# Kernel optimization log

Hardware: AMD Instinct MI355X
Metric: run time of the kernel (lower is better)

## Reference

```python
import jax, jax.numpy as jnp
import numpy as np

DIM_MODEL = 512
HEADS = 8
DIM_HEAD = 64
HIDDEN = HEADS * DIM_HEAD
SCALE = DIM_HEAD ** -0.5
GN_EPS = 1e-5


def setup_inputs() -> dict:
    key = jax.random.key(0)
    ks = jax.random.split(key, 7)
    b, t = 8, 4096
    x = jax.random.normal(ks[0], (b, DIM_MODEL, t), dtype=jnp.float32)
    mask = jax.random.randint(ks[1], (b, t), 0, 2) == 1  # bool padding mask
    # 1x1 convs are plain channel matmuls; kernels squeezed to 2D
    w_qkv = jax.random.normal(ks[2], (3 * HIDDEN, DIM_MODEL), dtype=jnp.float32) * (DIM_MODEL ** -0.5)
    w_out = jax.random.normal(ks[3], (DIM_MODEL, HIDDEN), dtype=jnp.float32) * (HIDDEN ** -0.5)
    b_out = jax.random.normal(ks[4], (DIM_MODEL,), dtype=jnp.float32) * 0.01
    gn_gamma = jnp.ones((DIM_MODEL,), dtype=jnp.float32)
    gn_beta = jnp.zeros((DIM_MODEL,), dtype=jnp.float32)
    return {"x": x, "mask": mask, "w_qkv": w_qkv, "w_out": w_out,
            "b_out": b_out, "gn_gamma": gn_gamma, "gn_beta": gn_beta}


def reference(x, mask, w_qkv, w_out, b_out, gn_gamma, gn_beta):
    b, c, t = x.shape
    # to_qkv: 1x1 conv == channel matmul -> [b, 3*hidden, t]
    qkv = jnp.einsum('oc,bct->bot', w_qkv, x)
    q, k, v = jnp.split(qkv, 3, axis=1)
    # 'b (h d) t -> b h d t'
    q = q.reshape(b, HEADS, DIM_HEAD, t)
    k = k.reshape(b, HEADS, DIM_HEAD, t)
    v = v.reshape(b, HEADS, DIM_HEAD, t)
    # additive mask: 0.0 where True, 1e-12 where False; broadcast 'b t -> b 1 1 t'
    maskf = jnp.where(mask, 0.0, 1e-12)[:, None, None, :].astype(x.dtype)
    q = jax.nn.softmax(q, axis=-2) * SCALE            # softmax over feature dim d
    k = jax.nn.softmax(k + maskf, axis=-1)            # softmax over time dim t
    # linear attention: O(t * d * e)
    context = jnp.einsum('bhdn,bhen->bhde', k, v)      # [b, h, d, e]
    out = jnp.einsum('bhde,bhdn->bhen', context, q)    # [b, h, e, t]
    out = out.reshape(b, HIDDEN, t)                    # 'b h e t -> b (h e) t'
    # to_out: 1x1 conv with bias, then GroupNorm(1, dim_model)
    y = jnp.einsum('oc,bct->bot', w_out, out) + b_out[None, :, None]
    mu = jnp.mean(y, axis=(1, 2), keepdims=True)
    var = jnp.var(y, axis=(1, 2), keepdims=True)
    y = (y - mu) * jax.lax.rsqrt(var + GN_EPS)
    return y * gn_gamma[None, :, None] + gn_beta[None, :, None]
```

## Files before the change

### kernel.cpp

```cpp
#include <hip/hip_runtime.h>
#include <stdint.h>

typedef unsigned short u16;
using f32x4 = __attribute__((ext_vector_type(4))) float;
using s16x8 = __attribute__((ext_vector_type(8))) short;

#define MFMA_BF16(a, b, c) __builtin_amdgcn_mfma_f32_16x16x32_bf16((a), (b), (c), 0, 0, 0)

#define GLOAD_LDS16(gptr, lptr)                                                               \
  __builtin_amdgcn_global_load_lds((const __attribute__((address_space(1))) uint32_t*)(gptr), \
                                   (__attribute__((address_space(3))) uint32_t*)(lptr), 16, 0, 0)

__device__ __forceinline__ u16 f2bf(float f) {
  union { float f; uint32_t u; } v; v.f = f;
  uint32_t r = v.u + 0x7fffu + ((v.u >> 16) & 1u);
  return (u16)(r >> 16);
}
__device__ __forceinline__ float bf2f(u16 h) {
  union { uint32_t u; float f; } v; v.u = ((uint32_t)h) << 16;
  return v.f;
}

__global__ void k_convert_w(const float* __restrict__ wq, const float* __restrict__ wo,
                            u16* __restrict__ wqb, u16* __restrict__ wob) {
  int i = blockIdx.x * 256 + threadIdx.x;
  const int nq = 1536 * 512 / 4;
  const int no = 512 * 512 / 4;
  if (i < nq) {
    float4 v = ((const float4*)wq)[i];
    u16* o = wqb + i * 4;
    o[0] = f2bf(v.x); o[1] = f2bf(v.y); o[2] = f2bf(v.z); o[3] = f2bf(v.w);
  } else if (i < nq + no) {
    int j = i - nq;
    float4 v = ((const float4*)wo)[j];
    u16* o = wob + j * 4;
    o[0] = f2bf(v.x); o[1] = f2bf(v.y); o[2] = f2bf(v.z); o[3] = f2bf(v.w);
  }
}

__global__ void k_transpose_x(const float* __restrict__ x, u16* __restrict__ xT) {
  __shared__ u16 tile[64][65];
  int b = blockIdx.z, c0 = blockIdx.y * 64, t0 = blockIdx.x * 64;
  const float* xp = x + ((size_t)b * 512 + c0) * 4096 + t0;
#pragma unroll
  for (int i = 0; i < 16; ++i) {
    int idx = threadIdx.x + i * 256;
    int r = idx >> 6, col = idx & 63;
    tile[r][col] = f2bf(xp[(size_t)r * 4096 + col]);
  }
  __syncthreads();
  u16* op = xT + ((size_t)b * 4096 + t0) * 512 + c0;
#pragma unroll
  for (int i = 0; i < 16; ++i) {
    int idx = threadIdx.x + i * 256;
    int r = idx >> 6, col = idx & 63;
    op[(size_t)r * 512 + col] = tile[col][r];
  }
}

__launch_bounds__(256, 2)
__global__ void k_gemm_qkv(const u16* __restrict__ A, const u16* __restrict__ BT,
                           u16* __restrict__ C, u16* __restrict__ qT) {
  __shared__ s16x8 As8[1024];
  __shared__ s16x8 Bs8[1024];
  int b = blockIdx.z;
  int m0 = blockIdx.y * 128, n0 = blockIdx.x * 128;
  const u16* Ab = A + (size_t)m0 * 512;
  const u16* Bb = BT + ((size_t)b * 4096 + n0) * 512;
  int tid = threadIdx.x, w = tid >> 6, lane = tid & 63;
  int wm = (w >> 1) * 64, wn = (w & 1) * 64;
  f32x4 acc[4][4] = {};
  for (int kt = 0; kt < 8; ++kt) {
    if (kt) __syncthreads();
#pragma unroll
    for (int it = 0; it < 4; ++it) {
      int L = (w * 4 + it) * 64 + lane;
      int r = L >> 3;
      int lc = (L & 7) ^ (r & 7);
      GLOAD_LDS16(Ab + (size_t)r * 512 + kt * 64 + lc * 8, ((char*)As8) + (w * 4 + it) * 1024);
      GLOAD_LDS16(Bb + (size_t)r * 512 + kt * 64 + lc * 8, ((char*)Bs8) + (w * 4 + it) * 1024);
    }
    asm volatile("s_waitcnt vmcnt(0)");
    __syncthreads();
#pragma unroll
    for (int kk = 0; kk < 2; ++kk) {
      int cb = kk * 4 + (lane >> 4);
      s16x8 af[4], bfr[4];
#pragma unroll
      for (int mi = 0; mi < 4; ++mi) {
        int r = wm + mi * 16 + (lane & 15);
        af[mi] = As8[r * 8 + (cb ^ (r & 7))];
      }
#pragma unroll
      for (int ni = 0; ni < 4; ++ni) {
        int r = wn + ni * 16 + (lane & 15);
        bfr[ni] = Bs8[r * 8 + (cb ^ (r & 7))];
      }
#pragma unroll
      for (int mi = 0; mi < 4; ++mi)
#pragma unroll
        for (int ni = 0; ni < 4; ++ni)
          acc[mi][ni] = MFMA_BF16(af[mi], bfr[ni], acc[mi][ni]);
    }
  }
  if (blockIdx.y < 4) {
    int head = (m0 >> 6) + (wm >> 6);
    int bh = b * 8 + head;
#pragma unroll
    for (int ni = 0; ni < 4; ++ni) {
      float mx = -1e30f;
#pragma unroll
      for (int mi = 0; mi < 4; ++mi)
#pragma unroll
        for (int j = 0; j < 4; ++j) mx = fmaxf(mx, acc[mi][ni][j]);
      mx = fmaxf(mx, __shfl_xor(mx, 16));
      mx = fmaxf(mx, __shfl_xor(mx, 32));
      float e[4][4];
      float s = 0.f;
#pragma unroll
      for (int mi = 0; mi < 4; ++mi)
#pragma unroll
        for (int j = 0; j < 4; ++j) { e[mi][j] = __expf(acc[mi][ni][j] - mx); s += e[mi][j]; }
      s += __shfl_xor(s, 16);
      s += __shfl_xor(s, 32);
      float sc = 0.125f / s;
      int t = n0 + wn + ni * 16 + (lane & 15);
      u16* op = qT + ((size_t)bh * 4096 + t) * 64 + (lane >> 4) * 4;
#pragma unroll
      for (int mi = 0; mi < 4; ++mi) {
        union { u16 u[4]; uint2 v; } pk;
#pragma unroll
        for (int j = 0; j < 4; ++j) pk.u[j] = f2bf(e[mi][j] * sc);
        *(uint2*)(op + mi * 16) = pk.v;
      }
    }
  } else {
    u16* Cb = C + ((size_t)b * 1536 + m0) * 4096 + n0;
#pragma unroll
    for (int mi = 0; mi < 4; ++mi)
#pragma unroll
      for (int ni = 0; ni < 4; ++ni)
#pragma unroll
        for (int j = 0; j < 4; ++j) {
          int mm = wm + mi * 16 + (lane >> 4) * 4 + j;
          int nn = wn + ni * 16 + (lane & 15);
          Cb[(size_t)mm * 4096 + nn] = f2bf(acc[mi][ni][j]);
        }
  }
}

__global__ void k_context_part(const u16* __restrict__ qkv, float* __restrict__ ctxp,
                               float* __restrict__ spart) {
  int s = blockIdx.x, bh = blockIdx.y;
  int b = bh >> 3, h = bh & 7;
  int w = threadIdx.x >> 6, lane = threadIdx.x & 63;
  int hi = lane >> 4, lo = lane & 15;
  const u16* vb = qkv + ((size_t)b * 1536 + 1024 + h * 64) * 4096 + s * 256;
  const u16* kb = qkv + ((size_t)b * 1536 + 512 + h * 64) * 4096 + s * 256;
  int d = w * 16 + lo;
  f32x4 acc[4] = {};
  float ssum = 0.f;
#pragma unroll
  for (int st = 0; st < 8; ++st) {
    int nn = st * 32 + hi * 8;
    s16x8 braw = *(const s16x8*)(kb + (size_t)d * 4096 + nn);
    s16x8 bexp;
#pragma unroll
    for (int j = 0; j < 8; ++j) {
      float f = __expf(bf2f((u16)braw[j]));
      ssum += f;
      bexp[j] = (short)f2bf(f);
    }
#pragma unroll
    for (int ei = 0; ei < 4; ++ei) {
      s16x8 a = *(const s16x8*)(vb + (size_t)(ei * 16 + lo) * 4096 + nn);
      acc[ei] = MFMA_BF16(a, bexp, acc[ei]);
    }
  }
  float* cp = ctxp + ((size_t)bh * 16 + s) * 4096;
#pragma unroll
  for (int ei = 0; ei < 4; ++ei) {
    float4 o;
    o.x = acc[ei][0]; o.y = acc[ei][1]; o.z = acc[ei][2]; o.w = acc[ei][3];
    *(float4*)&cp[(size_t)d * 64 + ei * 16 + hi * 4] = o;
  }
  ssum += __shfl_xor(ssum, 16);
  ssum += __shfl_xor(ssum, 32);
  if (lane < 16) spart[((size_t)bh * 16 + s) * 64 + w * 16 + lane] = ssum;
}

__global__ void k_ctx_reduce(const float* __restrict__ ctxp, const float* __restrict__ spart,
                             u16* __restrict__ Bg) {
  int q = blockIdx.x, bh = blockIdx.y;
  __shared__ float sinv[4];
  int tid = threadIdx.x;
  if (tid < 4) {
    int d = q * 4 + tid;
    float s = 0.f;
#pragma unroll
    for (int si = 0; si < 16; ++si) s += spart[((size_t)bh * 16 + si) * 64 + d];
    sinv[tid] = 1.f / s;
  }
  __syncthreads();
  int pos = q * 256 + tid;
  float v = 0.f;
#pragma unroll
  for (int si = 0; si < 16; ++si) v += ctxp[((size_t)bh * 16 + si) * 4096 + pos];
  Bg[(size_t)bh * 4096 + pos] = f2bf(v * sinv[(pos >> 6) & 3]);
}

__global__ void k_wfused(const u16* __restrict__ wout, const u16* __restrict__ Bg,
                         u16* __restrict__ Wf) {
  int bh = blockIdx.x;
  int b = bh >> 3, h = bh & 7;
  int w = threadIdx.x >> 6, lane = threadIdx.x & 63;
  int hi = lane >> 4, lo = lane & 15;
  const u16* Bb = Bg + (size_t)bh * 4096;
  const u16* Ab = wout + (size_t)h * 64;
  f32x4 acc[8][4] = {};
#pragma unroll
  for (int ks = 0; ks < 2; ++ks) {
    s16x8 bfr[4];
#pragma unroll
    for (int ni = 0; ni < 4; ++ni)
      bfr[ni] = *(const s16x8*)(Bb + (size_t)(ni * 16 + lo) * 64 + ks * 32 + hi * 8);
#pragma unroll
    for (int mi = 0; mi < 8; ++mi) {
      s16x8 a = *(const s16x8*)(Ab + (size_t)(w * 128 + mi * 16 + lo) * 512 + ks * 32 + hi * 8);
#pragma unroll
      for (int ni = 0; ni < 4; ++ni) acc[mi][ni] = MFMA_BF16(a, bfr[ni], acc[mi][ni]);
    }
  }
#pragma unroll
  for (int mi = 0; mi < 8; ++mi)
#pragma unroll
    for (int ni = 0; ni < 4; ++ni) {
      int m = w * 128 + mi * 16 + hi * 4;
      int d = ni * 16 + lo;
#pragma unroll
      for (int j = 0; j < 4; ++j)
        Wf[((size_t)b * 512 + m + j) * 512 + h * 64 + d] = f2bf(acc[mi][ni][j]);
    }
}

__launch_bounds__(256, 2)
__global__ void k_gemm_final(const u16* __restrict__ Wf, const u16* __restrict__ qT,
                             u16* __restrict__ Ybf, const float* __restrict__ bias,
                             float2* __restrict__ part2) {
  __shared__ s16x8 As8[1024];
  __shared__ s16x8 Bs8[1024];
  int b = blockIdx.z;
  int m0 = blockIdx.y * 128, n0 = blockIdx.x * 128;
  const u16* Ab = Wf + ((size_t)b * 512 + m0) * 512;
  const u16* qTb = qT + (size_t)b * 8 * 4096 * 64;
  int tid = threadIdx.x, w = tid >> 6, lane = tid & 63;
  int wm = (w >> 1) * 64, wn = (w & 1) * 64;
  f32x4 acc[4][4] = {};
  for (int kt = 0; kt < 8; ++kt) {
    if (kt) __syncthreads();
#pragma unroll
    for (int it = 0; it < 4; ++it) {
      int L = (w * 4 + it) * 64 + lane;
      int r = L >> 3;
      int lc = (L & 7) ^ (r & 7);
      GLOAD_LDS16(Ab + (size_t)r * 512 + kt * 64 + lc * 8, ((char*)As8) + (w * 4 + it) * 1024);
      int G = kt * 8 + lc;
      GLOAD_LDS16(qTb + ((size_t)(G >> 3) * 4096 + n0 + r) * 64 + (G & 7) * 8,
                  ((char*)Bs8) + (w * 4 + it) * 1024);
    }
    asm volatile("s_waitcnt vmcnt(0)");
    __syncthreads();
#pragma unroll
    for (int kk = 0; kk < 2; ++kk) {
      int cb = kk * 4 + (lane >> 4);
      s16x8 af[4], bfr[4];
#pragma unroll
      for (int mi = 0; mi < 4; ++mi) {
        int r = wm + mi * 16 + (lane & 15);
        af[mi] = As8[r * 8 + (cb ^ (r & 7))];
      }
#pragma unroll
      for (int ni = 0; ni < 4; ++ni) {
        int r = wn + ni * 16 + (lane & 15);
        bfr[ni] = Bs8[r * 8 + (cb ^ (r & 7))];
      }
#pragma unroll
      for (int mi = 0; mi < 4; ++mi)
#pragma unroll
        for (int ni = 0; ni < 4; ++ni)
          acc[mi][ni] = MFMA_BF16(af[mi], bfr[ni], acc[mi][ni]);
    }
  }
  u16* Yb = Ybf + ((size_t)b * 512 + m0) * 4096 + n0;
  float sm = 0.f, ssm = 0.f;
#pragma unroll
  for (int mi = 0; mi < 4; ++mi)
#pragma unroll
    for (int j = 0; j < 4; ++j) {
      int mm = wm + mi * 16 + (lane >> 4) * 4 + j;
      float bo = bias[m0 + mm];
#pragma unroll
      for (int ni = 0; ni < 4; ++ni) {
        int nn = wn + ni * 16 + (lane & 15);
        float vv = acc[mi][ni][j] + bo;
        sm += vv;
        ssm += vv * vv;
        Yb[(size_t)mm * 4096 + nn] = f2bf(vv);
      }
    }
#pragma unroll
  for (int off = 32; off; off >>= 1) { sm += __shfl_xor(sm, off); ssm += __shfl_xor(ssm, off); }
  __shared__ float sr[4], ssr[4];
  if (lane == 0) { sr[w] = sm; ssr[w] = ssm; }
  __syncthreads();
  if (tid == 0) {
    float2 o;
    o.x = sr[0] + sr[1] + sr[2] + sr[3];
    o.y = ssr[0] + ssr[1] + ssr[2] + ssr[3];
    part2[((size_t)b * 4 + blockIdx.y) * 32 + blockIdx.x] = o;
  }
}

__global__ void k_gn_norm(const u16* __restrict__ ybf, float* __restrict__ y,
                          const float2* __restrict__ part2,
                          const float* __restrict__ gamma, const float* __restrict__ beta) {
  int b = blockIdx.y;
  float s = 0.f, ss = 0.f;
#pragma unroll 8
  for (int i = 0; i < 128; ++i) { float2 pp = part2[b * 128 + i]; s += pp.x; ss += pp.y; }
  const float N = 512.f * 4096.f;
  float mu = s / N;
  float var = ss / N - mu * mu;
  float rstd = rsqrtf(var + 1e-5f);
  size_t base = ((size_t)b << 21) + (size_t)blockIdx.x * 16384;
  const s16x8* ip = (const s16x8*)(ybf + base);
  float4* opf = (float4*)(y + base);
#pragma unroll
  for (int i = 0; i < 8; ++i) {
    int idx = threadIdx.x + i * 256;
    int loc = (int)(blockIdx.x * 16384) + idx * 8;
    int c = loc >> 12;
    float g = gamma[c] * rstd, bt = beta[c];
    s16x8 v = ip[idx];
    float4 o0, o1;
    o0.x = (bf2f((u16)v[0]) - mu) * g + bt;
    o0.y = (bf2f((u16)v[1]) - mu) * g + bt;
    o0.z = (bf2f((u16)v[2]) - mu) * g + bt;
    o0.w = (bf2f((u16)v[3]) - mu) * g + bt;
    o1.x = (bf2f((u16)v[4]) - mu) * g + bt;
    o1.y = (bf2f((u16)v[5]) - mu) * g + bt;
    o1.z = (bf2f((u16)v[6]) - mu) * g + bt;
    o1.w = (bf2f((u16)v[7]) - mu) * g + bt;
    opf[idx * 2] = o0;
    opf[idx * 2 + 1] = o1;
  }
}

extern "C" void kernel_launch(void* const* d_in, const int* in_sizes, int n_in,
                              void* d_out, int out_size, void* d_ws, size_t ws_size,
                              hipStream_t stream) {
  const float* x     = (const float*)d_in[0];
  const float* wqkv  = (const float*)d_in[2];
  const float* wout  = (const float*)d_in[3];
  const float* bout  = (const float*)d_in[4];
  const float* gamma = (const float*)d_in[5];
  const float* beta  = (const float*)d_in[6];
  float* y = (float*)d_out;

  char* ws = (char*)d_ws;
  u16*    qkv_b = (u16*)ws;
  u16*    ybf   = (u16*)ws;
  u16*    xT    = (u16*)(ws + 100663296);
  float*  ctxp  = (float*)(ws + 100663296);
  float*  spart = (float*)(ws + 117440512);
  u16*    Bg    = (u16*)(ws + 117702656);
  u16*    qT    = (u16*)(ws + 134217728);
  u16*    wqkvb = (u16*)(ws + 167772160);
  u16*    woutb = (u16*)(ws + 169345024);
  u16*    Wfused= (u16*)(ws + 169869312);
  float2* part2 = (float2*)(ws + 174063616);

  k_convert_w<<<1024, 256, 0, stream>>>(wqkv, wout, wqkvb, woutb);
  {
    dim3 g(64, 8, 8);
    k_transpose_x<<<g, 256, 0, stream>>>(x, xT);
  }
  {
    dim3 g(32, 12, 8);
    k_gemm_qkv<<<g, 256, 0, stream>>>(wqkvb, xT, qkv_b, qT);
  }
  {
    dim3 g(16, 64);
    k_context_part<<<g, 256, 0, stream>>>(qkv_b, ctxp, spart);
  }
  {
    dim3 g(16, 64);
    k_ctx_reduce<<<g, 256, 0, stream>>>(ctxp, spart, Bg);
  }
  k_wfused<<<64, 256, 0, stream>>>(woutb, Bg, Wfused);
  {
    dim3 g(32, 4, 8);
    k_gemm_final<<<g, 256, 0, stream>>>(Wfused, qT, ybf, bout, part2);
  }
  {
    dim3 g(128, 8);
    k_gn_norm<<<g, 256, 0, stream>>>(ybf, y, part2, gamma, beta);
  }
}
```

Before: 177.9 us.

## Triple-buffer GEMM K-loop with 8-wave 128x256 tiles for QKV and final GEMMs

Replaces the synchronous single-buffer K loop in both big GEMMs with a shared macro that uses 8 waves, 128x256 output tiles and a three-stage LDS ring. Loads for tile kt+2 are issued while MFMAs run on tile kt, with s_setprio raised around the MFMA blocks. The aim is to hide global load latency and cut the wait-then-sync stalls. In exchange the kernels use 144KB of dynamic LDS, which allows only one block per CU, and the grid is halved, so the GroupNorm partial-sum count drops to 64 per batch.

```diff
diff --git a/kernel.cpp b/kernel.cpp
--- a/kernel.cpp
+++ b/kernel.cpp
@@ -58,53 +58,111 @@
   }
 }
 
-__launch_bounds__(256, 2)
+#define GEMM8W_CORE(ABASE, BSRC)                                                      \
+  s16x8* Asl = (s16x8*)lds;                             \
+  s16x8* Bsl = (s16x8*)(lds + 49152);                   \
+  int tid = threadIdx.x, w = tid >> 6, lane = tid & 63;                               \
+  int wr = w >> 2, wc = w & 3;                                                        \
+  int hi = lane >> 4, lo = lane & 15;                                                 \
+  int rsu = tid >> 3, pc = tid & 7;                                                   \
+  int lcs = pc ^ (rsu & 7);                                                           \
+  f32x4 acc[4][4] = {};                                                               \
+  _Pragma("unroll")                                                                   \
+  for (int t = 0; t < 2; ++t) {                                                       \
+    _Pragma("unroll")                                                                 \
+    for (int u = 0; u < 2; ++u) {                                                     \
+      int rr = u * 64 + rsu;                                                          \
+      GLOAD_LDS16(ABASE + (size_t)rr * 512 + t * 64 + lcs * 8,                        \
+                  ((char*)Asl) + ((size_t)t * 1024 + rr * 8 + pc) * 16);              \
+    }                                                                                 \
+    _Pragma("unroll")                                                                 \
+    for (int u = 0; u < 4; ++u) {                                                     \
+      int rr = u * 64 + rsu;                                                          \
+      GLOAD_LDS16(BSRC(rr, t, lcs),                                                   \
+                  ((char*)Bsl) + ((size_t)t * 2048 + rr * 8 + pc) * 16);              \
+    }                                                                                 \
+  }                                                                                   \
+  for (int kt = 0; kt < 8; ++kt) {                                                    \
+    if (kt < 7) { asm volatile("s_waitcnt vmcnt(6)" ::: "memory"); }                  \
+    else        { asm volatile("s_waitcnt vmcnt(0)" ::: "memory"); }                  \
+    __builtin_amdgcn_s_barrier();                                                     \
+    int bufc = kt % 3, bufs = (kt + 2) % 3;                                           \
+    const s16x8* Ac = Asl + bufc * 1024;                                              \
+    const s16x8* Bc = Bsl + bufc * 2048;                                              \
+    bool st = (kt < 6);                                                               \
+    s16x8 af[4], bfr[4];                                                              \
+    _Pragma("unroll")                                                                 \
+    for (int mi = 0; mi < 4; ++mi) {                                                  \
+      int r = wr * 64 + mi * 16 + lo;                                                 \
+      af[mi] = Ac[r * 8 + (hi ^ (r & 7))];                                            \
+    }                                                                                 \
+    _Pragma("unroll")                                                                 \
+    for (int ni = 0; ni < 4; ++ni) {                                                  \
+      int r = wc * 64 + ni * 16 + lo;                                                 \
+      bfr[ni] = Bc[r * 8 + (hi ^ (r & 7))];                                           \
+    }                                                                                 \
+    if (st) {                                                                         \
+      _Pragma("unroll")                                                               \
+      for (int u = 0; u < 2; ++u) {                                                   \
+        int rr = u * 64 + rsu;                                                        \
+        GLOAD_LDS16(ABASE + (size_t)rr * 512 + (kt + 2) * 64 + lcs * 8,               \
+                    ((char*)Asl) + ((size_t)bufs * 1024 + rr * 8 + pc) * 16);         \
+      }                                                                               \
+      {                                                                               \
+        int rr = rsu;                                                                 \
+        GLOAD_LDS16(BSRC(rr, (kt + 2), lcs),                                          \
+                    ((char*)Bsl) + ((size_t)bufs * 2048 + rr * 8 + pc) * 16);         \
+      }                                                                               \
+    }                                                                                 \
+    __builtin_amdgcn_s_setprio(1);                                                    \
+    _Pragma("unroll")                                                                 \
+    for (int mi = 0; mi < 4; ++mi)                                                    \
+      _Pragma("unroll")                                                               \
+      for (int ni = 0; ni < 4; ++ni)                                                  \
+        acc[mi][ni] = MFMA_BF16(af[mi], bfr[ni], acc[mi][ni]);                        \
+    __builtin_amdgcn_s_setprio(0);                                                    \
+    __builtin_amdgcn_s_barrier();                                                     \
+    _Pragma("unroll")                                                                 \
+    for (int mi = 0; mi < 4; ++mi) {                                                  \
+      int r = wr * 64 + mi * 16 + lo;                                                 \
+      af[mi] = Ac[r * 8 + ((4 + hi) ^ (r & 7))];                                      \
+    }                                                                                 \
+    _Pragma("unroll")                                                                 \
+    for (int ni = 0; ni < 4; ++ni) {                                                  \
+      int r = wc * 64 + ni * 16 + lo;                                                 \
+      bfr[ni] = Bc[r * 8 + ((4 + hi) ^ (r & 7))];                                     \
+    }                                                                                 \
+    if (st) {                                                                         \
+      _Pragma("unroll")                                                               \
+      for (int u = 1; u < 4; ++u) {                                                   \
+        int rr = u * 64 + rsu;                                                        \
+        GLOAD_LDS16(BSRC(rr, (kt + 2), lcs),                                          \
+                    ((char*)Bsl) + ((size_t)bufs * 2048 + rr * 8 + pc) * 16);         \
+      }                                                                               \
+    }                                                                                 \
+    __builtin_amdgcn_s_setprio(1);                                                    \
+    _Pragma("unroll")                                                                 \
+    for (int mi = 0; mi < 4; ++mi)                                                    \
+      _Pragma("unroll")                                                               \
+      for (int ni = 0; ni < 4; ++ni)                                                  \
+        acc[mi][ni] = MFMA_BF16(af[mi], bfr[ni], acc[mi][ni]);                        \
+    __builtin_amdgcn_s_setprio(0);                                                    \
+  }
+
+#define BSRC_X(rr, ktile, lc) (Bb + (size_t)(rr) * 512 + (ktile) * 64 + (lc) * 8)
+#define BSRC_Q(rr, ktile, lc) (Bq + (size_t)(ktile) * 262144 + (size_t)(rr) * 64 + (lc) * 8)
+
+__launch_bounds__(512, 1)
 __global__ void k_gemm_qkv(const u16* __restrict__ A, const u16* __restrict__ BT,
                            u16* __restrict__ C, u16* __restrict__ qT) {
-  __shared__ s16x8 As8[1024];
-  __shared__ s16x8 Bs8[1024];
+  extern __shared__ char lds[];
   int b = blockIdx.z;
-  int m0 = blockIdx.y * 128, n0 = blockIdx.x * 128;
+  int m0 = blockIdx.y * 128, n0 = blockIdx.x * 256;
   const u16* Ab = A + (size_t)m0 * 512;
   const u16* Bb = BT + ((size_t)b * 4096 + n0) * 512;
-  int tid = threadIdx.x, w = tid >> 6, lane = tid & 63;
-  int wm = (w >> 1) * 64, wn = (w & 1) * 64;
-  f32x4 acc[4][4] = {};
-  for (int kt = 0; kt < 8; ++kt) {
-    if (kt) __syncthreads();
-#pragma unroll
-    for (int it = 0; it < 4; ++it) {
-      int L = (w * 4 + it) * 64 + lane;
-      int r = L >> 3;
-      int lc = (L & 7) ^ (r & 7);
-      GLOAD_LDS16(Ab + (size_t)r * 512 + kt * 64 + lc * 8, ((char*)As8) + (w * 4 + it) * 1024);
-      GLOAD_LDS16(Bb + (size_t)r * 512 + kt * 64 + lc * 8, ((char*)Bs8) + (w * 4 + it) * 1024);
-    }
-    asm volatile("s_waitcnt vmcnt(0)");
-    __syncthreads();
-#pragma unroll
-    for (int kk = 0; kk < 2; ++kk) {
-      int cb = kk * 4 + (lane >> 4);
-      s16x8 af[4], bfr[4];
-#pragma unroll
-      for (int mi = 0; mi < 4; ++mi) {
-        int r = wm + mi * 16 + (lane & 15);
-        af[mi] = As8[r * 8 + (cb ^ (r & 7))];
-      }
-#pragma unroll
-      for (int ni = 0; ni < 4; ++ni) {
-        int r = wn + ni * 16 + (lane & 15);
-        bfr[ni] = Bs8[r * 8 + (cb ^ (r & 7))];
-      }
-#pragma unroll
-      for (int mi = 0; mi < 4; ++mi)
-#pragma unroll
-        for (int ni = 0; ni < 4; ++ni)
-          acc[mi][ni] = MFMA_BF16(af[mi], bfr[ni], acc[mi][ni]);
-    }
-  }
+  GEMM8W_CORE(Ab, BSRC_X)
   if (blockIdx.y < 4) {
-    int head = (m0 >> 6) + (wm >> 6);
+    int head = (int)blockIdx.y * 2 + wr;
     int bh = b * 8 + head;
 #pragma unroll
     for (int ni = 0; ni < 4; ++ni) {
@@ -124,8 +182,8 @@
       s += __shfl_xor(s, 16);
       s += __shfl_xor(s, 32);
       float sc = 0.125f / s;
-      int t = n0 + wn + ni * 16 + (lane & 15);
-      u16* op = qT + ((size_t)bh * 4096 + t) * 64 + (lane >> 4) * 4;
+      int t = n0 + wc * 64 + ni * 16 + lo;
+      u16* op = qT + ((size_t)bh * 4096 + t) * 64 + hi * 4;
 #pragma unroll
       for (int mi = 0; mi < 4; ++mi) {
         union { u16 u[4]; uint2 v; } pk;
@@ -142,10 +200,53 @@
       for (int ni = 0; ni < 4; ++ni)
 #pragma unroll
         for (int j = 0; j < 4; ++j) {
-          int mm = wm + mi * 16 + (lane >> 4) * 4 + j;
-          int nn = wn + ni * 16 + (lane & 15);
+          int mm = wr * 64 + mi * 16 + hi * 4 + j;
+          int nn = wc * 64 + ni * 16 + lo;
           Cb[(size_t)mm * 4096 + nn] = f2bf(acc[mi][ni][j]);
         }
+  }
+}
+
+__launch_bounds__(512, 1)
+__global__ void k_gemm_final(const u16* __restrict__ Wf, const u16* __restrict__ qT,
+                             u16* __restrict__ Ybf, const float* __restrict__ bias,
+                             float2* __restrict__ part2) {
+  extern __shared__ char lds[];
+  int b = blockIdx.z;
+  int m0 = blockIdx.y * 128, n0 = blockIdx.x * 256;
+  const u16* Ab = Wf + ((size_t)b * 512 + m0) * 512;
+  const u16* Bq = qT + ((size_t)b * 8 * 4096 + n0) * 64;
+  GEMM8W_CORE(Ab, BSRC_Q)
+  u16* Yb = Ybf + ((size_t)b * 512 + m0) * 4096 + n0;
+  float sm = 0.f, ssm = 0.f;
+#pragma unroll
+  for (int mi = 0; mi < 4; ++mi)
+#pragma unroll
+    for (int j = 0; j < 4; ++j) {
+      int mm = wr * 64 + mi * 16 + hi * 4 + j;
+      float bo = bias[m0 + mm];
+#pragma unroll
+      for (int ni = 0; ni < 4; ++ni) {
+        int nn = wc * 64 + ni * 16 + lo;
+        float vv = acc[mi][ni][j] + bo;
+        sm += vv;
+        ssm += vv * vv;
+        Yb[(size_t)mm * 4096 + nn] = f2bf(vv);
+      }
+    }
+#pragma unroll
+  for (int off = 32; off; off >>= 1) { sm += __shfl_xor(sm, off); ssm += __shfl_xor(ssm, off); }
+  float* sr = (float*)lds;
+  float* ssr = sr + 8;
+  __syncthreads();
+  if (lane == 0) { sr[w] = sm; ssr[w] = ssm; }
+  __syncthreads();
+  if (tid == 0) {
+    float2 o;
+    o.x = 0.f; o.y = 0.f;
+#pragma unroll
+    for (int i = 0; i < 8; ++i) { o.x += sr[i]; o.y += ssr[i]; }
+    part2[((size_t)b * 4 + blockIdx.y) * 16 + blockIdx.x] = o;
   }
 }
 
@@ -243,91 +344,13 @@
     }
 }
 
-__launch_bounds__(256, 2)
-__global__ void k_gemm_final(const u16* __restrict__ Wf, const u16* __restrict__ qT,
-                             u16* __restrict__ Ybf, const float* __restrict__ bias,
-                             float2* __restrict__ part2) {
-  __shared__ s16x8 As8[1024];
-  __shared__ s16x8 Bs8[1024];
-  int b = blockIdx.z;
-  int m0 = blockIdx.y * 128, n0 = blockIdx.x * 128;
-  const u16* Ab = Wf + ((size_t)b * 512 + m0) * 512;
-  const u16* qTb = qT + (size_t)b * 8 * 4096 * 64;
-  int tid = threadIdx.x, w = tid >> 6, lane = tid & 63;
-  int wm = (w >> 1) * 64, wn = (w & 1) * 64;
-  f32x4 acc[4][4] = {};
-  for (int kt = 0; kt < 8; ++kt) {
-    if (kt) __syncthreads();
-#pragma unroll
-    for (int it = 0; it < 4; ++it) {
-      int L = (w * 4 + it) * 64 + lane;
-      int r = L >> 3;
-      int lc = (L & 7) ^ (r & 7);
-      GLOAD_LDS16(Ab + (size_t)r * 512 + kt * 64 + lc * 8, ((char*)As8) + (w * 4 + it) * 1024);
-      int G = kt * 8 + lc;
-      GLOAD_LDS16(qTb + ((size_t)(G >> 3) * 4096 + n0 + r) * 64 + (G & 7) * 8,
-                  ((char*)Bs8) + (w * 4 + it) * 1024);
-    }
-    asm volatile("s_waitcnt vmcnt(0)");
-    __syncthreads();
-#pragma unroll
-    for (int kk = 0; kk < 2; ++kk) {
-      int cb = kk * 4 + (lane >> 4);
-      s16x8 af[4], bfr[4];
-#pragma unroll
-      for (int mi = 0; mi < 4; ++mi) {
-        int r = wm + mi * 16 + (lane & 15);
-        af[mi] = As8[r * 8 + (cb ^ (r & 7))];
-      }
-#pragma unroll
-      for (int ni = 0; ni < 4; ++ni) {
-        int r = wn + ni * 16 + (lane & 15);
-        bfr[ni] = Bs8[r * 8 + (cb ^ (r & 7))];
-      }
-#pragma unroll
-      for (int mi = 0; mi < 4; ++mi)
-#pragma unroll
-        for (int ni = 0; ni < 4; ++ni)
-          acc[mi][ni] = MFMA_BF16(af[mi], bfr[ni], acc[mi][ni]);
-    }
-  }
-  u16* Yb = Ybf + ((size_t)b * 512 + m0) * 4096 + n0;
-  float sm = 0.f, ssm = 0.f;
-#pragma unroll
-  for (int mi = 0; mi < 4; ++mi)
-#pragma unroll
-    for (int j = 0; j < 4; ++j) {
-      int mm = wm + mi * 16 + (lane >> 4) * 4 + j;
-      float bo = bias[m0 + mm];
-#pragma unroll
-      for (int ni = 0; ni < 4; ++ni) {
-        int nn = wn + ni * 16 + (lane & 15);
-        float vv = acc[mi][ni][j] + bo;
-        sm += vv;
-        ssm += vv * vv;
-        Yb[(size_t)mm * 4096 + nn] = f2bf(vv);
-      }
-    }
-#pragma unroll
-  for (int off = 32; off; off >>= 1) { sm += __shfl_xor(sm, off); ssm += __shfl_xor(ssm, off); }
-  __shared__ float sr[4], ssr[4];
-  if (lane == 0) { sr[w] = sm; ssr[w] = ssm; }
-  __syncthreads();
-  if (tid == 0) {
-    float2 o;
-    o.x = sr[0] + sr[1] + sr[2] + sr[3];
-    o.y = ssr[0] + ssr[1] + ssr[2] + ssr[3];
-    part2[((size_t)b * 4 + blockIdx.y) * 32 + blockIdx.x] = o;
-  }
-}
-
 __global__ void k_gn_norm(const u16* __restrict__ ybf, float* __restrict__ y,
                           const float2* __restrict__ part2,
                           const float* __restrict__ gamma, const float* __restrict__ beta) {
   int b = blockIdx.y;
   float s = 0.f, ss = 0.f;
 #pragma unroll 8
-  for (int i = 0; i < 128; ++i) { float2 pp = part2[b * 128 + i]; s += pp.x; ss += pp.y; }
+  for (int i = 0; i < 64; ++i) { float2 pp = part2[b * 64 + i]; s += pp.x; ss += pp.y; }
   const float N = 512.f * 4096.f;
   float mu = s / N;
   float var = ss / N - mu * mu;
@@ -380,14 +403,20 @@
   u16*    Wfused= (u16*)(ws + 169869312);
   float2* part2 = (float2*)(ws + 174063616);
 
+  const int GEMM_LDS = 147456;
+  (void)hipFuncSetAttribute((const void*)k_gemm_qkv,
+                            hipFuncAttributeMaxDynamicSharedMemorySize, GEMM_LDS);
+  (void)hipFuncSetAttribute((const void*)k_gemm_final,
+                            hipFuncAttributeMaxDynamicSharedMemorySize, GEMM_LDS);
+
   k_convert_w<<<1024, 256, 0, stream>>>(wqkv, wout, wqkvb, woutb);
   {
     dim3 g(64, 8, 8);
     k_transpose_x<<<g, 256, 0, stream>>>(x, xT);
   }
   {
-    dim3 g(32, 12, 8);
-    k_gemm_qkv<<<g, 256, 0, stream>>>(wqkvb, xT, qkv_b, qT);
+    dim3 g(16, 12, 8);
+    k_gemm_qkv<<<g, 512, GEMM_LDS, stream>>>(wqkvb, xT, qkv_b, qT);
   }
   {
     dim3 g(16, 64);
@@ -399,8 +428,8 @@
   }
   k_wfused<<<64, 256, 0, stream>>>(woutb, Bg, Wfused);
   {
-    dim3 g(32, 4, 8);
-    k_gemm_final<<<g, 256, 0, stream>>>(Wfused, qT, ybf, bout, part2);
+    dim3 g(16, 4, 8);
+    k_gemm_final<<<g, 512, GEMM_LDS, stream>>>(Wfused, qT, ybf, bout, part2);
   }
   {
     dim3 g(128, 8);
```

Result: no change. 176.3 us (-0.9%).

## Fuse K-exp and K·V context into QKV GEMM epilogue, merge reduce with wfused

Applied to the files above, without the earlier changes.

The QKV GEMM blocks for K/V now load the matching K and V head rows together, so the epilogue can exponentiate K, stage exp(K) and V in LDS and compute partial K·V^T context per 128-token slice directly. This removes the bf16 K/V write to global memory and the separate context kernel's reread. The context reduction and the w_out fusion are merged into one kernel that sums 32 partials in place of 16. The cost is a larger LDS footprint, an extra sync and more partial buffers to reduce, with only 64 blocks doing that reduction.

```diff
diff --git a/kernel.cpp b/kernel.cpp
--- a/kernel.cpp
+++ b/kernel.cpp
@@ -60,14 +60,25 @@
 
 __launch_bounds__(256, 2)
 __global__ void k_gemm_qkv(const u16* __restrict__ A, const u16* __restrict__ BT,
-                           u16* __restrict__ C, u16* __restrict__ qT) {
-  __shared__ s16x8 As8[1024];
-  __shared__ s16x8 Bs8[1024];
+                           u16* __restrict__ qT, float* __restrict__ ctxp,
+                           float* __restrict__ spart) {
+  __shared__ __align__(16) char ldsbuf[35328];
+  s16x8* As8 = (s16x8*)ldsbuf;
+  s16x8* Bs8 = (s16x8*)(ldsbuf + 16384);
   int b = blockIdx.z;
   int m0 = blockIdx.y * 128, n0 = blockIdx.x * 128;
-  const u16* Ab = A + (size_t)m0 * 512;
+  const u16 *Ab0, *Ab1;
+  if (blockIdx.y < 4) {
+    Ab0 = A + (size_t)m0 * 512;
+    Ab1 = A + (size_t)(m0 + 64) * 512;
+  } else {
+    int h = (int)blockIdx.y - 4;
+    Ab0 = A + (size_t)(512 + h * 64) * 512;
+    Ab1 = A + (size_t)(1024 + h * 64) * 512;
+  }
   const u16* Bb = BT + ((size_t)b * 4096 + n0) * 512;
   int tid = threadIdx.x, w = tid >> 6, lane = tid & 63;
+  int hi = lane >> 4, lo = lane & 15;
   int wm = (w >> 1) * 64, wn = (w & 1) * 64;
   f32x4 acc[4][4] = {};
   for (int kt = 0; kt < 8; ++kt) {
@@ -77,23 +88,25 @@
       int L = (w * 4 + it) * 64 + lane;
       int r = L >> 3;
       int lc = (L & 7) ^ (r & 7);
-      GLOAD_LDS16(Ab + (size_t)r * 512 + kt * 64 + lc * 8, ((char*)As8) + (w * 4 + it) * 1024);
+      const u16* abase = ((w * 4 + it) < 8) ? Ab0 : Ab1;
+      int rr = r & 63;
+      GLOAD_LDS16(abase + (size_t)rr * 512 + kt * 64 + lc * 8, ((char*)As8) + (w * 4 + it) * 1024);
       GLOAD_LDS16(Bb + (size_t)r * 512 + kt * 64 + lc * 8, ((char*)Bs8) + (w * 4 + it) * 1024);
     }
     asm volatile("s_waitcnt vmcnt(0)");
     __syncthreads();
 #pragma unroll
     for (int kk = 0; kk < 2; ++kk) {
-      int cb = kk * 4 + (lane >> 4);
+      int cb = kk * 4 + hi;
       s16x8 af[4], bfr[4];
 #pragma unroll
       for (int mi = 0; mi < 4; ++mi) {
-        int r = wm + mi * 16 + (lane & 15);
+        int r = wm + mi * 16 + lo;
         af[mi] = As8[r * 8 + (cb ^ (r & 7))];
       }
 #pragma unroll
       for (int ni = 0; ni < 4; ++ni) {
-        int r = wn + ni * 16 + (lane & 15);
+        int r = wn + ni * 16 + lo;
         bfr[ni] = Bs8[r * 8 + (cb ^ (r & 7))];
       }
 #pragma unroll
@@ -103,6 +116,7 @@
           acc[mi][ni] = MFMA_BF16(af[mi], bfr[ni], acc[mi][ni]);
     }
   }
+  __syncthreads();
   if (blockIdx.y < 4) {
     int head = (m0 >> 6) + (wm >> 6);
     int bh = b * 8 + head;
@@ -124,8 +138,8 @@
       s += __shfl_xor(s, 16);
       s += __shfl_xor(s, 32);
       float sc = 0.125f / s;
-      int t = n0 + wn + ni * 16 + (lane & 15);
-      u16* op = qT + ((size_t)bh * 4096 + t) * 64 + (lane >> 4) * 4;
+      int t = n0 + wn + ni * 16 + lo;
+      u16* op = qT + ((size_t)bh * 4096 + t) * 64 + hi * 4;
 #pragma unroll
       for (int mi = 0; mi < 4; ++mi) {
         union { u16 u[4]; uint2 v; } pk;
@@ -135,87 +149,99 @@
       }
     }
   } else {
-    u16* Cb = C + ((size_t)b * 1536 + m0) * 4096 + n0;
-#pragma unroll
-    for (int mi = 0; mi < 4; ++mi)
-#pragma unroll
-      for (int ni = 0; ni < 4; ++ni)
+    int h = (int)blockIdx.y - 4;
+    int bh = b * 8 + h;
+    int s = blockIdx.x;
+    u16* ekl = (u16*)ldsbuf;
+    u16* vtl = (u16*)(ldsbuf + 17408);
+    float* sums = (float*)(ldsbuf + 34816);
+    if (wm == 0) {
+      float rsum[4][4];
+#pragma unroll
+      for (int mi = 0; mi < 4; ++mi)
 #pragma unroll
         for (int j = 0; j < 4; ++j) {
-          int mm = wm + mi * 16 + (lane >> 4) * 4 + j;
-          int nn = wn + ni * 16 + (lane & 15);
-          Cb[(size_t)mm * 4096 + nn] = f2bf(acc[mi][ni][j]);
+          float t = 0.f;
+#pragma unroll
+          for (int ni = 0; ni < 4; ++ni) {
+            float e = __expf(acc[mi][ni][j]);
+            ekl[(mi * 16 + hi * 4 + j) * 136 + wn + ni * 16 + lo] = f2bf(e);
+            t += e;
+          }
+          rsum[mi][j] = t;
         }
-  }
-}
-
-__global__ void k_context_part(const u16* __restrict__ qkv, float* __restrict__ ctxp,
-                               float* __restrict__ spart) {
-  int s = blockIdx.x, bh = blockIdx.y;
-  int b = bh >> 3, h = bh & 7;
-  int w = threadIdx.x >> 6, lane = threadIdx.x & 63;
-  int hi = lane >> 4, lo = lane & 15;
-  const u16* vb = qkv + ((size_t)b * 1536 + 1024 + h * 64) * 4096 + s * 256;
-  const u16* kb = qkv + ((size_t)b * 1536 + 512 + h * 64) * 4096 + s * 256;
-  int d = w * 16 + lo;
-  f32x4 acc[4] = {};
-  float ssum = 0.f;
-#pragma unroll
-  for (int st = 0; st < 8; ++st) {
-    int nn = st * 32 + hi * 8;
-    s16x8 braw = *(const s16x8*)(kb + (size_t)d * 4096 + nn);
-    s16x8 bexp;
-#pragma unroll
-    for (int j = 0; j < 8; ++j) {
-      float f = __expf(bf2f((u16)braw[j]));
-      ssum += f;
-      bexp[j] = (short)f2bf(f);
-    }
-#pragma unroll
-    for (int ei = 0; ei < 4; ++ei) {
-      s16x8 a = *(const s16x8*)(vb + (size_t)(ei * 16 + lo) * 4096 + nn);
-      acc[ei] = MFMA_BF16(a, bexp, acc[ei]);
-    }
-  }
-  float* cp = ctxp + ((size_t)bh * 16 + s) * 4096;
-#pragma unroll
-  for (int ei = 0; ei < 4; ++ei) {
-    float4 o;
-    o.x = acc[ei][0]; o.y = acc[ei][1]; o.z = acc[ei][2]; o.w = acc[ei][3];
-    *(float4*)&cp[(size_t)d * 64 + ei * 16 + hi * 4] = o;
-  }
-  ssum += __shfl_xor(ssum, 16);
-  ssum += __shfl_xor(ssum, 32);
-  if (lane < 16) spart[((size_t)bh * 16 + s) * 64 + w * 16 + lane] = ssum;
-}
-
-__global__ void k_ctx_reduce(const float* __restrict__ ctxp, const float* __restrict__ spart,
-                             u16* __restrict__ Bg) {
-  int q = blockIdx.x, bh = blockIdx.y;
-  __shared__ float sinv[4];
-  int tid = threadIdx.x;
-  if (tid < 4) {
-    int d = q * 4 + tid;
-    float s = 0.f;
-#pragma unroll
-    for (int si = 0; si < 16; ++si) s += spart[((size_t)bh * 16 + si) * 64 + d];
-    sinv[tid] = 1.f / s;
-  }
-  __syncthreads();
-  int pos = q * 256 + tid;
-  float v = 0.f;
-#pragma unroll
-  for (int si = 0; si < 16; ++si) v += ctxp[((size_t)bh * 16 + si) * 4096 + pos];
-  Bg[(size_t)bh * 4096 + pos] = f2bf(v * sinv[(pos >> 6) & 3]);
-}
-
-__global__ void k_wfused(const u16* __restrict__ wout, const u16* __restrict__ Bg,
-                         u16* __restrict__ Wf) {
+#pragma unroll
+      for (int mi = 0; mi < 4; ++mi)
+#pragma unroll
+        for (int j = 0; j < 4; ++j) {
+#pragma unroll
+          for (int msk = 1; msk <= 8; msk <<= 1) rsum[mi][j] += __shfl_xor(rsum[mi][j], msk);
+        }
+      if (lo == 0) {
+#pragma unroll
+        for (int mi = 0; mi < 4; ++mi)
+#pragma unroll
+          for (int j = 0; j < 4; ++j) sums[(w & 1) * 64 + mi * 16 + hi * 4 + j] = rsum[mi][j];
+      }
+    } else {
+#pragma unroll
+      for (int mi = 0; mi < 4; ++mi)
+#pragma unroll
+        for (int j = 0; j < 4; ++j)
+#pragma unroll
+          for (int ni = 0; ni < 4; ++ni)
+            vtl[(mi * 16 + hi * 4 + j) * 136 + wn + ni * 16 + lo] = f2bf(acc[mi][ni][j]);
+    }
+    __syncthreads();
+    int d0 = w * 16;
+    f32x4 c2[4] = {};
+#pragma unroll
+    for (int kk = 0; kk < 4; ++kk) {
+      s16x8 ae = *(const s16x8*)&ekl[(d0 + lo) * 136 + kk * 32 + hi * 8];
+#pragma unroll
+      for (int ni = 0; ni < 4; ++ni) {
+        s16x8 bv = *(const s16x8*)&vtl[(ni * 16 + lo) * 136 + kk * 32 + hi * 8];
+        c2[ni] = MFMA_BF16(ae, bv, c2[ni]);
+      }
+    }
+    float* cp = ctxp + ((size_t)bh * 32 + s) * 4096;
+#pragma unroll
+    for (int ni = 0; ni < 4; ++ni)
+#pragma unroll
+      for (int j = 0; j < 4; ++j)
+        cp[(size_t)(d0 + hi * 4 + j) * 64 + ni * 16 + lo] = c2[ni][j];
+    if (w == 0) {
+      spart[((size_t)bh * 32 + s) * 64 + lane] = sums[lane] + sums[64 + lane];
+    }
+  }
+}
+
+__global__ void k_ctx_wfused(const float* __restrict__ ctxp, const float* __restrict__ spart,
+                             const u16* __restrict__ wout, u16* __restrict__ Wf) {
+  __shared__ float sinv[64];
+  __shared__ __align__(16) u16 Bgl[64 * 72];
   int bh = blockIdx.x;
   int b = bh >> 3, h = bh & 7;
-  int w = threadIdx.x >> 6, lane = threadIdx.x & 63;
-  int hi = lane >> 4, lo = lane & 15;
-  const u16* Bb = Bg + (size_t)bh * 4096;
+  int tid = threadIdx.x;
+  if (tid < 64) {
+    float ssum = 0.f;
+#pragma unroll 8
+    for (int s = 0; s < 32; ++s) ssum += spart[((size_t)bh * 32 + s) * 64 + tid];
+    sinv[tid] = 1.f / ssum;
+  }
+  __syncthreads();
+  const float* cb = ctxp + (size_t)bh * 32 * 4096;
+#pragma unroll
+  for (int i = 0; i < 16; ++i) {
+    int pos = i * 256 + tid;
+    float v = 0.f;
+#pragma unroll 8
+    for (int s = 0; s < 32; ++s) v += cb[(size_t)s * 4096 + pos];
+    int d = pos >> 6, e = pos & 63;
+    Bgl[d * 72 + e] = f2bf(v * sinv[d]);
+  }
+  __syncthreads();
+  int w = tid >> 6, lane = tid & 63, hi = lane >> 4, lo = lane & 15;
   const u16* Ab = wout + (size_t)h * 64;
   f32x4 acc[8][4] = {};
 #pragma unroll
@@ -223,7 +249,7 @@
     s16x8 bfr[4];
 #pragma unroll
     for (int ni = 0; ni < 4; ++ni)
-      bfr[ni] = *(const s16x8*)(Bb + (size_t)(ni * 16 + lo) * 64 + ks * 32 + hi * 8);
+      bfr[ni] = *(const s16x8*)&Bgl[(ni * 16 + lo) * 72 + ks * 32 + hi * 8];
 #pragma unroll
     for (int mi = 0; mi < 8; ++mi) {
       s16x8 a = *(const s16x8*)(Ab + (size_t)(w * 128 + mi * 16 + lo) * 512 + ks * 32 + hi * 8);
@@ -368,17 +394,15 @@
   float* y = (float*)d_out;
 
   char* ws = (char*)d_ws;
-  u16*    qkv_b = (u16*)ws;
   u16*    ybf   = (u16*)ws;
-  u16*    xT    = (u16*)(ws + 100663296);
-  float*  ctxp  = (float*)(ws + 100663296);
-  float*  spart = (float*)(ws + 117440512);
-  u16*    Bg    = (u16*)(ws + 117702656);
-  u16*    qT    = (u16*)(ws + 134217728);
-  u16*    wqkvb = (u16*)(ws + 167772160);
-  u16*    woutb = (u16*)(ws + 169345024);
-  u16*    Wfused= (u16*)(ws + 169869312);
-  float2* part2 = (float2*)(ws + 174063616);
+  u16*    qT    = (u16*)(ws + 33554432);
+  float*  ctxp  = (float*)(ws + 67108864);
+  float*  spart = (float*)(ws + 100663296);
+  u16*    wqkvb = (u16*)(ws + 101187584);
+  u16*    woutb = (u16*)(ws + 102760448);
+  u16*    Wfused= (u16*)(ws + 103284736);
+  float2* part2 = (float2*)(ws + 107479040);
+  u16*    xT    = (u16*)(ws + 107487232);
 
   k_convert_w<<<1024, 256, 0, stream>>>(wqkv, wout, wqkvb, woutb);
   {
@@ -387,17 +411,9 @@
   }
   {
     dim3 g(32, 12, 8);
-    k_gemm_qkv<<<g, 256, 0, stream>>>(wqkvb, xT, qkv_b, qT);
-  }
-  {
-    dim3 g(16, 64);
-    k_context_part<<<g, 256, 0, stream>>>(qkv_b, ctxp, spart);
-  }
-  {
-    dim3 g(16, 64);
-    k_ctx_reduce<<<g, 256, 0, stream>>>(ctxp, spart, Bg);
-  }
-  k_wfused<<<64, 256, 0, stream>>>(woutb, Bg, Wfused);
+    k_gemm_qkv<<<g, 256, 0, stream>>>(wqkvb, xT, qT, ctxp, spart);
+  }
+  k_ctx_wfused<<<64, 256, 0, stream>>>(ctxp, spart, woutb, Wfused);
   {
     dim3 g(32, 4, 8);
     k_gemm_final<<<g, 256, 0, stream>>>(Wfused, qT, ybf, bout, part2);
```

Measured after the change: 185.5 us. 4.2% more time.

## Fuse weight conversion into transpose, move k-exp and row sums into QKV GEMM epilogue

Applied to the files above, without the earlier changes.

Folds the weight fp32-to-bf16 conversion into an extra z-slice of the transpose launch, removing one kernel launch. The transpose now uses float4 loads and 16-byte vectorized stores. The exp of k and its per-row partial sums move into the QKV GEMM epilogue, written as 32 partials per row. The context kernel then reads pre-exponentiated k directly and the reduce sums the new partial layout. The cost is extra epilogue work, a shared-memory reduction with a block barrier in the GEMM, and no max-subtraction before the exp of k, which matches the prior code.

```diff
diff --git a/kernel.cpp b/kernel.cpp
--- a/kernel.cpp
+++ b/kernel.cpp
@@ -21,48 +21,60 @@
   return v.f;
 }
 
-__global__ void k_convert_w(const float* __restrict__ wq, const float* __restrict__ wo,
-                            u16* __restrict__ wqb, u16* __restrict__ wob) {
-  int i = blockIdx.x * 256 + threadIdx.x;
-  const int nq = 1536 * 512 / 4;
-  const int no = 512 * 512 / 4;
-  if (i < nq) {
-    float4 v = ((const float4*)wq)[i];
-    u16* o = wqb + i * 4;
-    o[0] = f2bf(v.x); o[1] = f2bf(v.y); o[2] = f2bf(v.z); o[3] = f2bf(v.w);
-  } else if (i < nq + no) {
-    int j = i - nq;
-    float4 v = ((const float4*)wo)[j];
-    u16* o = wob + j * 4;
-    o[0] = f2bf(v.x); o[1] = f2bf(v.y); o[2] = f2bf(v.z); o[3] = f2bf(v.w);
-  }
-}
-
-__global__ void k_transpose_x(const float* __restrict__ x, u16* __restrict__ xT) {
-  __shared__ u16 tile[64][65];
+__global__ void k_transpose_x(const float* __restrict__ x, u16* __restrict__ xT,
+                              const float* __restrict__ wq, const float* __restrict__ wo,
+                              u16* __restrict__ wqb, u16* __restrict__ wob) {
+  if (blockIdx.z == 8) {
+    const int nq = 1536 * 512 / 4;
+    const int no = 512 * 512 / 4;
+    int bid = blockIdx.y * 64 + blockIdx.x;
+#pragma unroll
+    for (int rep = 0; rep < 2; ++rep) {
+      int i = bid * 256 + threadIdx.x + rep * 131072;
+      if (i < nq) {
+        float4 v = ((const float4*)wq)[i];
+        u16* o = wqb + i * 4;
+        o[0] = f2bf(v.x); o[1] = f2bf(v.y); o[2] = f2bf(v.z); o[3] = f2bf(v.w);
+      } else if (i < nq + no) {
+        int j = i - nq;
+        float4 v = ((const float4*)wo)[j];
+        u16* o = wob + j * 4;
+        o[0] = f2bf(v.x); o[1] = f2bf(v.y); o[2] = f2bf(v.z); o[3] = f2bf(v.w);
+      }
+    }
+    return;
+  }
+  __shared__ u16 tile[64][68];
   int b = blockIdx.z, c0 = blockIdx.y * 64, t0 = blockIdx.x * 64;
   const float* xp = x + ((size_t)b * 512 + c0) * 4096 + t0;
 #pragma unroll
-  for (int i = 0; i < 16; ++i) {
-    int idx = threadIdx.x + i * 256;
-    int r = idx >> 6, col = idx & 63;
-    tile[r][col] = f2bf(xp[(size_t)r * 4096 + col]);
+  for (int it = 0; it < 4; ++it) {
+    int r = it * 16 + (threadIdx.x >> 4), c4 = (threadIdx.x & 15) * 4;
+    float4 v = *(const float4*)(xp + (size_t)r * 4096 + c4);
+    tile[r][c4 + 0] = f2bf(v.x);
+    tile[r][c4 + 1] = f2bf(v.y);
+    tile[r][c4 + 2] = f2bf(v.z);
+    tile[r][c4 + 3] = f2bf(v.w);
   }
   __syncthreads();
   u16* op = xT + ((size_t)b * 4096 + t0) * 512 + c0;
 #pragma unroll
-  for (int i = 0; i < 16; ++i) {
-    int idx = threadIdx.x + i * 256;
-    int r = idx >> 6, col = idx & 63;
-    op[(size_t)r * 512 + col] = tile[col][r];
+  for (int it = 0; it < 2; ++it) {
+    int tr = it * 32 + (threadIdx.x >> 3), cb = (threadIdx.x & 7) * 8;
+    s16x8 o;
+#pragma unroll
+    for (int jj = 0; jj < 8; ++jj) o[jj] = tile[cb + jj][tr];
+    *(s16x8*)(op + (size_t)tr * 512 + cb) = o;
   }
 }
 
 __launch_bounds__(256, 2)
 __global__ void k_gemm_qkv(const u16* __restrict__ A, const u16* __restrict__ BT,
-                           u16* __restrict__ C, u16* __restrict__ qT) {
+                           u16* __restrict__ C, u16* __restrict__ qT,
+                           float* __restrict__ spart) {
   __shared__ s16x8 As8[1024];
   __shared__ s16x8 Bs8[1024];
+  __shared__ float ksums[4][64];
   int b = blockIdx.z;
   int m0 = blockIdx.y * 128, n0 = blockIdx.x * 128;
   const u16* Ab = A + (size_t)m0 * 512;
@@ -134,6 +146,33 @@
         *(uint2*)(op + mi * 16) = pk.v;
       }
     }
+  } else if (blockIdx.y < 8) {
+    u16* Cb = C + ((size_t)b * 1536 + m0) * 4096 + n0;
+#pragma unroll
+    for (int mi = 0; mi < 4; ++mi)
+#pragma unroll
+      for (int j = 0; j < 4; ++j) {
+        int mm = wm + mi * 16 + (lane >> 4) * 4 + j;
+        float t = 0.f;
+#pragma unroll
+        for (int ni = 0; ni < 4; ++ni) {
+          int nn = wn + ni * 16 + (lane & 15);
+          float e = __expf(acc[mi][ni][j]);
+          t += e;
+          Cb[(size_t)mm * 4096 + nn] = f2bf(e);
+        }
+        t += __shfl_xor(t, 1);
+        t += __shfl_xor(t, 2);
+        t += __shfl_xor(t, 4);
+        t += __shfl_xor(t, 8);
+        if ((lane & 15) == 0) ksums[w][mi * 16 + (lane >> 4) * 4 + j] = t;
+      }
+    __syncthreads();
+    if (tid < 128) {
+      int hr = tid >> 6, r = tid & 63;
+      float v = ksums[hr * 2][r] + ksums[hr * 2 + 1][r];
+      spart[((size_t)b * 512 + (m0 - 512) + hr * 64 + r) * 32 + blockIdx.x] = v;
+    }
   } else {
     u16* Cb = C + ((size_t)b * 1536 + m0) * 4096 + n0;
 #pragma unroll
@@ -149,8 +188,7 @@
   }
 }
 
-__global__ void k_context_part(const u16* __restrict__ qkv, float* __restrict__ ctxp,
-                               float* __restrict__ spart) {
+__global__ void k_context_part(const u16* __restrict__ qkv, float* __restrict__ ctxp) {
   int s = blockIdx.x, bh = blockIdx.y;
   int b = bh >> 3, h = bh & 7;
   int w = threadIdx.x >> 6, lane = threadIdx.x & 63;
@@ -159,18 +197,10 @@
   const u16* kb = qkv + ((size_t)b * 1536 + 512 + h * 64) * 4096 + s * 256;
   int d = w * 16 + lo;
   f32x4 acc[4] = {};
-  float ssum = 0.f;
 #pragma unroll
   for (int st = 0; st < 8; ++st) {
     int nn = st * 32 + hi * 8;
-    s16x8 braw = *(const s16x8*)(kb + (size_t)d * 4096 + nn);
-    s16x8 bexp;
-#pragma unroll
-    for (int j = 0; j < 8; ++j) {
-      float f = __expf(bf2f((u16)braw[j]));
-      ssum += f;
-      bexp[j] = (short)f2bf(f);
-    }
+    s16x8 bexp = *(const s16x8*)(kb + (size_t)d * 4096 + nn);
 #pragma unroll
     for (int ei = 0; ei < 4; ++ei) {
       s16x8 a = *(const s16x8*)(vb + (size_t)(ei * 16 + lo) * 4096 + nn);
@@ -184,21 +214,20 @@
     o.x = acc[ei][0]; o.y = acc[ei][1]; o.z = acc[ei][2]; o.w = acc[ei][3];
     *(float4*)&cp[(size_t)d * 64 + ei * 16 + hi * 4] = o;
   }
-  ssum += __shfl_xor(ssum, 16);
-  ssum += __shfl_xor(ssum, 32);
-  if (lane < 16) spart[((size_t)bh * 16 + s) * 64 + w * 16 + lane] = ssum;
 }
 
 __global__ void k_ctx_reduce(const float* __restrict__ ctxp, const float* __restrict__ spart,
                              u16* __restrict__ Bg) {
   int q = blockIdx.x, bh = blockIdx.y;
+  int b = bh >> 3, h = bh & 7;
   __shared__ float sinv[4];
   int tid = threadIdx.x;
   if (tid < 4) {
-    int d = q * 4 + tid;
+    int hd = h * 64 + q * 4 + tid;
+    const float* sp = spart + ((size_t)b * 512 + hd) * 32;
     float s = 0.f;
 #pragma unroll
-    for (int si = 0; si < 16; ++si) s += spart[((size_t)bh * 16 + si) * 64 + d];
+    for (int xx = 0; xx < 32; ++xx) s += sp[xx];
     sinv[tid] = 1.f / s;
   }
   __syncthreads();
@@ -372,26 +401,25 @@
   u16*    ybf   = (u16*)ws;
   u16*    xT    = (u16*)(ws + 100663296);
   float*  ctxp  = (float*)(ws + 100663296);
-  float*  spart = (float*)(ws + 117440512);
   u16*    Bg    = (u16*)(ws + 117702656);
   u16*    qT    = (u16*)(ws + 134217728);
   u16*    wqkvb = (u16*)(ws + 167772160);
   u16*    woutb = (u16*)(ws + 169345024);
   u16*    Wfused= (u16*)(ws + 169869312);
   float2* part2 = (float2*)(ws + 174063616);
-
-  k_convert_w<<<1024, 256, 0, stream>>>(wqkv, wout, wqkvb, woutb);
-  {
-    dim3 g(64, 8, 8);
-    k_transpose_x<<<g, 256, 0, stream>>>(x, xT);
+  float*  spart = (float*)(ws + 174071808);
+
+  {
+    dim3 g(64, 8, 9);
+    k_transpose_x<<<g, 256, 0, stream>>>(x, xT, wqkv, wout, wqkvb, woutb);
   }
   {
     dim3 g(32, 12, 8);
-    k_gemm_qkv<<<g, 256, 0, stream>>>(wqkvb, xT, qkv_b, qT);
+    k_gemm_qkv<<<g, 256, 0, stream>>>(wqkvb, xT, qkv_b, qT, spart);
   }
   {
     dim3 g(16, 64);
-    k_context_part<<<g, 256, 0, stream>>>(qkv_b, ctxp, spart);
+    k_context_part<<<g, 256, 0, stream>>>(qkv_b, ctxp);
   }
   {
     dim3 g(16, 64);
```

After: 174.8 us. No clear change (-1.7%).
